# Kernel tuning notes

Hardware: AMD Instinct MI355X
Metric: run time of the kernel (lower is better)

The kernel has to match this reference:

```python
import jax, jax.numpy as jnp
import numpy as np

TAU = 0.5
EPS = 1e-12


def _projection(z, W1, b1, W2, b2):
    # fc2(elu(fc1(z)))
    h = jax.nn.elu(z @ W1 + b1)
    return h @ W2 + b2


def _l2_normalize(z):
    n = jnp.linalg.norm(z, axis=1, keepdims=True)
    return z / jnp.maximum(n, EPS)


def _semi_loss(h1, h2, tau):
    n1 = _l2_normalize(h1)
    n2 = _l2_normalize(h2)
    refl = jnp.exp((n1 @ n1.T) / tau)      # [N, N]
    between = jnp.exp((n1 @ n2.T) / tau)   # [N, N]
    denom = refl.sum(axis=1) + between.sum(axis=1) - jnp.diagonal(refl)
    return -jnp.log(jnp.diagonal(between) / denom)


def setup_inputs() -> dict:
    key = jax.random.key(0)
    k1, k2, k3, k4 = jax.random.split(key, 4)
    N, H, P = 12288, 256, 256
    s = 1.0 / np.sqrt(H)
    return {
        "z1": jax.random.normal(k1, (N, H), dtype=jnp.float32),
        "z2": jax.random.normal(k2, (N, H), dtype=jnp.float32),
        "W1": jax.random.normal(k3, (H, P), dtype=jnp.float32) * s,
        "b1": jnp.zeros((P,), dtype=jnp.float32),
        "W2": jax.random.normal(k4, (P, H), dtype=jnp.float32) * s,
        "b2": jnp.zeros((H,), dtype=jnp.float32),
    }


def reference(z1, z2, W1, b1, W2, b2):
    h1 = _projection(z1, W1, b1, W2, b2)
    h2 = _projection(z2, W1, b1, W2, b2)
    l1 = _semi_loss(h1, h2, TAU)
    l2 = _semi_loss(h2, h1, TAU)
    return ((l1 + l2) * 0.5).mean()
```

## Files before the change

### kernel.cpp

```cpp
#include <hip/hip_runtime.h>
#include <hip/hip_bf16.h>

typedef __attribute__((ext_vector_type(4))) float f32x4;
typedef __attribute__((ext_vector_type(8))) short bf16x8;

#define NR 12288
#define HD 256
#define TAU 0.5f
#define NU 24576
#define NTT 192
#define NSUB 384
#define NBLK (NTT * (NTT + 1) / 2)

__device__ __forceinline__ unsigned short f2bf(float f) {
    unsigned int x = __builtin_bit_cast(unsigned int, f);
    x += 0x7fffu + ((x >> 16) & 1u);
    return (unsigned short)(x >> 16);
}

__device__ __forceinline__ unsigned char f2e4m3(float f) {
    unsigned int u = __builtin_bit_cast(unsigned int, f);
    unsigned int s = (u >> 24) & 0x80u;
    float af = fabsf(f);
    if (af >= 464.f) return (unsigned char)(s | 0x7Eu);
    if (af < 0.015625f) {
        unsigned int q = (unsigned int)(af * 512.f + 0.5f);
        return (unsigned char)(s | q);
    }
    int e = (int)((u >> 23) & 0xffu) - 127;
    unsigned int mant = u & 0x7fffffu;
    unsigned int val = (unsigned int)((e + 7) << 3) | (mant >> 20);
    unsigned int rem = mant & 0xfffffu;
    val += (rem > 0x80000u) || (rem == 0x80000u && (val & 1u));
    return (unsigned char)(s | val);
}

__device__ __forceinline__ float row16_sum(float x) {
    int v;
    v = __builtin_amdgcn_update_dpp(0, __builtin_bit_cast(int, x), 0xB1, 0xF, 0xF, true);
    x += __builtin_bit_cast(float, v);
    v = __builtin_amdgcn_update_dpp(0, __builtin_bit_cast(int, x), 0x4E, 0xF, 0xF, true);
    x += __builtin_bit_cast(float, v);
    v = __builtin_amdgcn_update_dpp(0, __builtin_bit_cast(int, x), 0x141, 0xF, 0xF, true);
    x += __builtin_bit_cast(float, v);
    v = __builtin_amdgcn_update_dpp(0, __builtin_bit_cast(int, x), 0x140, 0xF, 0xF, true);
    x += __builtin_bit_cast(float, v);
    return x;
}

__global__ __launch_bounds__(256) void cast4_kernel(const float* __restrict__ src,
                                                    unsigned short* __restrict__ dst, int n4) {
    int i = blockIdx.x * 256 + threadIdx.x;
    if (i >= n4) return;
    float4 v = ((const float4*)src)[i];
    ushort4 u;
    u.x = f2bf(v.x); u.y = f2bf(v.y); u.z = f2bf(v.z); u.w = f2bf(v.w);
    ((ushort4*)dst)[i] = u;
}

__global__ __launch_bounds__(256) void transpose_cast_kernel(const float* __restrict__ W,
                                                             unsigned short* __restrict__ Wt) {
    int n = blockIdx.x;
    int k = threadIdx.x;
    Wt[n * HD + k] = f2bf(W[k * HD + n]);
}

template <int ELU>
__global__ __launch_bounds__(256) void proj_kernel(const unsigned short* __restrict__ A,
                                                   const unsigned short* __restrict__ Bt,
                                                   const float* __restrict__ bias,
                                                   void* __restrict__ Cout) {
    const int lane = threadIdx.x & 63;
    const int wave = threadIdx.x >> 6;
    const int row0 = blockIdx.x * 64;
    const int col0 = wave * 64;
    const int lr = lane & 15, lk = lane >> 4;

    f32x4 acc[4][4] = {};
    const unsigned short* Ab = A + (size_t)(row0 + lr) * HD + lk * 8;
    const unsigned short* Bb = Bt + (size_t)(col0 + lr) * HD + lk * 8;
#pragma unroll
    for (int k0 = 0; k0 < HD; k0 += 32) {
        bf16x8 af[4], bfr[4];
#pragma unroll
        for (int m = 0; m < 4; ++m) af[m] = *(const bf16x8*)(Ab + m * 16 * HD + k0);
#pragma unroll
        for (int n = 0; n < 4; ++n) bfr[n] = *(const bf16x8*)(Bb + n * 16 * HD + k0);
#pragma unroll
        for (int m = 0; m < 4; ++m)
#pragma unroll
            for (int n = 0; n < 4; ++n)
                acc[m][n] = __builtin_amdgcn_mfma_f32_16x16x32_bf16(af[m], bfr[n], acc[m][n], 0, 0, 0);
    }
#pragma unroll
    for (int m = 0; m < 4; ++m) {
#pragma unroll
        for (int n = 0; n < 4; ++n) {
            int col = col0 + n * 16 + lr;
            float b = bias[col];
#pragma unroll
            for (int r = 0; r < 4; ++r) {
                int row = row0 + m * 16 + lk * 4 + r;
                float v = acc[m][n][r] + b;
                if (ELU) {
                    v = v > 0.f ? v : expm1f(v);
                    ((unsigned short*)Cout)[(size_t)row * HD + col] = f2bf(v);
                } else {
                    ((float*)Cout)[(size_t)row * HD + col] = v;
                }
            }
        }
    }
}

__global__ __launch_bounds__(256) void norm_diag_kernel(const float* __restrict__ h1,
                                                        const float* __restrict__ h2,
                                                        unsigned char* __restrict__ n1,
                                                        unsigned char* __restrict__ n2,
                                                        float* __restrict__ dvec) {
    const int lane = threadIdx.x & 63;
    const int wave = threadIdx.x >> 6;
    const int row = blockIdx.x * 4 + wave;
    const float4 a = *(const float4*)(h1 + (size_t)row * HD + lane * 4);
    const float4 b = *(const float4*)(h2 + (size_t)row * HD + lane * 4);
    float sa = a.x * a.x + a.y * a.y + a.z * a.z + a.w * a.w;
    float sb = b.x * b.x + b.y * b.y + b.z * b.z + b.w * b.w;
    float sab = a.x * b.x + a.y * b.y + a.z * b.z + a.w * b.w;
#pragma unroll
    for (int m = 32; m; m >>= 1) {
        sa += __shfl_xor(sa, m);
        sb += __shfl_xor(sb, m);
        sab += __shfl_xor(sab, m);
    }
    float na = sqrtf(sa); na = na > 1e-12f ? na : 1e-12f;
    float nb = sqrtf(sb); nb = nb > 1e-12f ? nb : 1e-12f;
    float ia = 1.f / na, ib = 1.f / nb;
    uchar4 q1, q2;
    q1.x = f2e4m3(a.x * ia); q1.y = f2e4m3(a.y * ia); q1.z = f2e4m3(a.z * ia); q1.w = f2e4m3(a.w * ia);
    q2.x = f2e4m3(b.x * ib); q2.y = f2e4m3(b.y * ib); q2.z = f2e4m3(b.z * ib); q2.w = f2e4m3(b.w * ib);
    const int sw = ((row >> 3) & 1) << 3;
    *(uchar4*)(n1 + (size_t)row * HD + ((lane * 4) ^ sw)) = q1;
    *(uchar4*)(n2 + (size_t)row * HD + ((lane * 4) ^ sw)) = q2;
    if (lane == 0) dvec[row] = sab * ia * ib * (1.f / TAU);
}

__global__ __launch_bounds__(256, 2) void gram_kernel(const unsigned char* __restrict__ nU8,
                                                      float* __restrict__ RPART) {
    __shared__ __align__(16) unsigned char lA[128 * 256];
    __shared__ __align__(16) unsigned char lB[128 * 256];

    const int bid = blockIdx.x;
    const int t0 = (bid & 7) * (NBLK / 8) + (bid >> 3);
    int i = (int)((385.f - sqrtf((float)(385 * 385 - 8 * t0))) * 0.5f);
    if (i < 0) i = 0;
    if (i > NTT - 1) i = NTT - 1;
    while (i > 0 && i * NTT - i * (i - 1) / 2 > t0) --i;
    while ((i + 1) * NTT - (i + 1) * i / 2 <= t0) ++i;
    const int j = i + (t0 - (i * NTT - i * (i - 1) / 2));
    const bool diag = (i == j);

    const unsigned char* X = nU8 + (size_t)i * 128 * HD;
    const unsigned char* Y = nU8 + (size_t)j * 128 * HD;

    const int t = threadIdx.x;
    const int lane = t & 63;
    const int wave = t >> 6;
    const int wr = wave >> 1, wc = wave & 1;
    const int lr = lane & 15, lk = lane >> 4;

    {
        const int rbase = t >> 4;
        const int schunk = (t & 15) ^ rbase;
        const unsigned char* gx = X + rbase * 256 + schunk * 16;
        const unsigned char* gy = Y + rbase * 256 + schunk * 16;
#pragma unroll
        for (int c = 0; c < 8; ++c) {
            __builtin_amdgcn_global_load_lds(
                (const __attribute__((address_space(1))) unsigned int*)(gx + c * 4096),
                (__attribute__((address_space(3))) unsigned int*)(&lA[c * 4096 + t * 16]),
                16, 0, 0);
        }
        if (!diag) {
#pragma unroll
            for (int c = 0; c < 8; ++c) {
                __builtin_amdgcn_global_load_lds(
                    (const __attribute__((address_space(1))) unsigned int*)(gy + c * 4096),
                    (__attribute__((address_space(3))) unsigned int*)(&lB[c * 4096 + t * 16]),
                    16, 0, 0);
            }
        }
    }
    __syncthreads();

    f32x4 acc[4][4] = {};
    const int hswap = (lr >> 3) & 1;
    const unsigned char* sA = lA + (size_t)(wr * 64 + lr) * 256 + ((lk & 1) ^ hswap) * 8;
    const unsigned char* sBb = (diag ? lA : lB);
    const unsigned char* sB = sBb + (size_t)(wc * 64 + lr) * 256 + ((lk & 1) ^ hswap) * 8;
#pragma unroll
    for (int ks = 0; ks < 8; ++ks) {
        const int chnk = ((2 * ks + (lk >> 1)) ^ lr) * 16;
        long af[4], bfr[4];
#pragma unroll
        for (int m = 0; m < 4; ++m)
            af[m] = *(const long*)(sA + m * 16 * 256 + chnk);
#pragma unroll
        for (int n = 0; n < 4; ++n)
            bfr[n] = *(const long*)(sB + n * 16 * 256 + chnk);
#pragma unroll
        for (int m = 0; m < 4; ++m)
#pragma unroll
            for (int n = 0; n < 4; ++n)
                acc[m][n] = __builtin_amdgcn_mfma_f32_16x16x32_fp8_fp8(af[m], bfr[n], acc[m][n], 0, 0, 0);
    }

    const float kexp = 2.8853901f;
#pragma unroll
    for (int m = 0; m < 4; ++m)
#pragma unroll
        for (int n = 0; n < 4; ++n)
#pragma unroll
            for (int r = 0; r < 4; ++r)
                acc[m][n][r] = exp2f(acc[m][n][r] * kexp);

    {
        float* dst = RPART + (size_t)(2 * j + wc) * NU + i * 128 + wr * 64;
#pragma unroll
        for (int m = 0; m < 4; ++m) {
#pragma unroll
            for (int r = 0; r < 4; ++r) {
                float rs = (acc[m][0][r] + acc[m][1][r]) + (acc[m][2][r] + acc[m][3][r]);
                rs = row16_sum(rs);
                if (lr == 0) dst[m * 16 + lk * 4 + r] = rs;
            }
        }
    }
    if (!diag) {
        float* dst = RPART + (size_t)(2 * i + wr) * NU + j * 128 + wc * 64;
#pragma unroll
        for (int n = 0; n < 4; ++n) {
            float cs = 0.f;
#pragma unroll
            for (int m = 0; m < 4; ++m)
#pragma unroll
                for (int r = 0; r < 4; ++r) cs += acc[m][n][r];
            cs += __shfl_xor(cs, 16);
            cs += __shfl_xor(cs, 32);
            if (lk == 0) dst[n * 16 + lr] = cs;
        }
    }
}

__global__ __launch_bounds__(256) void reduce_part_kernel(const float* __restrict__ RPART,
                                                          float* __restrict__ S) {
    const int r = blockIdx.x * 256 + threadIdx.x;
    float s = 0.f;
#pragma unroll 8
    for (int p = 0; p < NSUB; ++p) s += RPART[(size_t)p * NU + r];
    S[r] = s;
}

__global__ __launch_bounds__(128) void loss_partial_kernel(const float* __restrict__ S,
                                                           const float* __restrict__ dvec,
                                                           float* __restrict__ partial) {
    int i = blockIdx.x * 128 + threadIdx.x;
    const float e2 = 7.389056099f;
    float d = dvec[i];
    float l1 = logf(S[i] - e2) - d;
    float l2 = logf(S[NR + i] - e2) - d;
    float v = 0.5f * (l1 + l2);
#pragma unroll
    for (int m = 32; m; m >>= 1) v += __shfl_xor(v, m);
    __shared__ float wsum[2];
    if ((threadIdx.x & 63) == 0) wsum[threadIdx.x >> 6] = v;
    __syncthreads();
    if (threadIdx.x == 0) partial[blockIdx.x] = wsum[0] + wsum[1];
}

__global__ __launch_bounds__(128) void loss_final_kernel(const float* __restrict__ partial,
                                                         float* __restrict__ out, int nb) {
    float s = 0.f;
    for (int i = threadIdx.x; i < nb; i += 128) s += partial[i];
#pragma unroll
    for (int m = 32; m; m >>= 1) s += __shfl_xor(s, m);
    __shared__ float wsum[2];
    if ((threadIdx.x & 63) == 0) wsum[threadIdx.x >> 6] = s;
    __syncthreads();
    if (threadIdx.x == 0) out[0] = (wsum[0] + wsum[1]) * (1.f / (float)NR);
}

extern "C" void kernel_launch(void* const* d_in, const int* in_sizes, int n_in,
                              void* d_out, int out_size, void* d_ws, size_t ws_size,
                              hipStream_t stream) {
    const float* z1 = (const float*)d_in[0];
    const float* z2 = (const float*)d_in[1];
    const float* W1 = (const float*)d_in[2];
    const float* b1 = (const float*)d_in[3];
    const float* W2 = (const float*)d_in[4];
    const float* b2 = (const float*)d_in[5];

    char* ws = (char*)d_ws;
    size_t off = 0;
    auto alloc = [&](size_t bytes) {
        void* p = ws + off;
        off += (bytes + 255) & ~(size_t)255;
        return p;
    };
    const size_t NH2 = (size_t)NR * HD * 2;
    unsigned short* zb1 = (unsigned short*)alloc(NH2);
    unsigned short* zb2 = (unsigned short*)alloc(NH2);
    unsigned short* W1t = (unsigned short*)alloc(HD * HD * 2);
    unsigned short* W2t = (unsigned short*)alloc(HD * HD * 2);
    unsigned short* t1 = (unsigned short*)alloc(NH2);
    unsigned short* t2 = (unsigned short*)alloc(NH2);
    float* h1 = (float*)alloc((size_t)NR * HD * 4);
    float* h2 = (float*)alloc((size_t)NR * HD * 4);
    unsigned char* nU = (unsigned char*)alloc((size_t)NU * HD);
    float* S = (float*)alloc((size_t)NU * 4);
    float* dvec = (float*)alloc(NR * 4);
    float* partial = (float*)alloc(96 * 4);
    float* RPART = (float*)ws;

    const int n4 = NR * HD / 4;
    cast4_kernel<<<(n4 + 255) / 256, 256, 0, stream>>>(z1, zb1, n4);
    cast4_kernel<<<(n4 + 255) / 256, 256, 0, stream>>>(z2, zb2, n4);
    transpose_cast_kernel<<<HD, 256, 0, stream>>>(W1, W1t);
    transpose_cast_kernel<<<HD, 256, 0, stream>>>(W2, W2t);

    proj_kernel<1><<<NR / 64, 256, 0, stream>>>(zb1, W1t, b1, t1);
    proj_kernel<1><<<NR / 64, 256, 0, stream>>>(zb2, W1t, b1, t2);
    proj_kernel<0><<<NR / 64, 256, 0, stream>>>(t1, W2t, b2, h1);
    proj_kernel<0><<<NR / 64, 256, 0, stream>>>(t2, W2t, b2, h2);

    norm_diag_kernel<<<NR / 4, 256, 0, stream>>>(h1, h2, nU, nU + (size_t)NR * HD, dvec);

    hipMemsetAsync(RPART, 0, (size_t)NSUB * NU * 4, stream);

    gram_kernel<<<NBLK, 256, 0, stream>>>(nU, RPART);

    reduce_part_kernel<<<NU / 256, 256, 0, stream>>>(RPART, S);

    loss_partial_kernel<<<NR / 128, 128, 0, stream>>>(S, dvec, partial);
    loss_final_kernel<<<1, 128, 0, stream>>>(partial, (float*)d_out, NR / 128);
}
```

Measured before the change: 293.7 us.

## Fuse cast, two-layer projection, normalization and fp8 quantization into one kernel

Replaces the two input casts, four projection GEMMs and the norm/diag kernel with one kernel per 64-row tile. It converts fp32 inputs to bf16 on the fly, keeps the ELU intermediate in swizzled LDS, and computes the norms, diagonal and fp8 quantization from registers, so the intermediate tensors never go through global memory. It also folds the exp scale into the quantization factor (sqrt of 2/(tau·ln2)), drops the RPART memset, and merges the reduce and loss-partial kernels. The trade-offs are higher register pressure (launch bounds 1), a narrower fp8 range for the pre-scaled values, and unzeroed RPART, which is only safe if the gram kernel writes every slot.

```diff
diff --git a/kernel.cpp b/kernel.cpp
--- a/kernel.cpp
+++ b/kernel.cpp
@@ -11,6 +11,7 @@
 #define NTT 192
 #define NSUB 384
 #define NBLK (NTT * (NTT + 1) / 2)
+#define LAM 1.69864368f
 
 __device__ __forceinline__ unsigned short f2bf(float f) {
     unsigned int x = __builtin_bit_cast(unsigned int, f);
@@ -48,14 +49,15 @@
     return x;
 }
 
-__global__ __launch_bounds__(256) void cast4_kernel(const float* __restrict__ src,
-                                                    unsigned short* __restrict__ dst, int n4) {
-    int i = blockIdx.x * 256 + threadIdx.x;
-    if (i >= n4) return;
-    float4 v = ((const float4*)src)[i];
-    ushort4 u;
-    u.x = f2bf(v.x); u.y = f2bf(v.y); u.z = f2bf(v.z); u.w = f2bf(v.w);
-    ((ushort4*)dst)[i] = u;
+__device__ __forceinline__ bf16x8 cvt8(const float* __restrict__ p) {
+    float4 a = *(const float4*)p;
+    float4 b = *(const float4*)(p + 4);
+    union { unsigned int i[4]; bf16x8 v; } u;
+    u.i[0] = ((unsigned int)f2bf(a.y) << 16) | f2bf(a.x);
+    u.i[1] = ((unsigned int)f2bf(a.w) << 16) | f2bf(a.z);
+    u.i[2] = ((unsigned int)f2bf(b.y) << 16) | f2bf(b.x);
+    u.i[3] = ((unsigned int)f2bf(b.w) << 16) | f2bf(b.z);
+    return u.v;
 }
 
 __global__ __launch_bounds__(256) void transpose_cast_kernel(const float* __restrict__ W,
@@ -65,83 +67,147 @@
     Wt[n * HD + k] = f2bf(W[k * HD + n]);
 }
 
-template <int ELU>
-__global__ __launch_bounds__(256) void proj_kernel(const unsigned short* __restrict__ A,
-                                                   const unsigned short* __restrict__ Bt,
-                                                   const float* __restrict__ bias,
-                                                   void* __restrict__ Cout) {
-    const int lane = threadIdx.x & 63;
-    const int wave = threadIdx.x >> 6;
+__global__ __launch_bounds__(256, 1) void fused_proj_kernel(const float* __restrict__ z1,
+                                                            const float* __restrict__ z2,
+                                                            const unsigned short* __restrict__ W1t,
+                                                            const unsigned short* __restrict__ W2t,
+                                                            const float* __restrict__ b1,
+                                                            const float* __restrict__ b2,
+                                                            unsigned char* __restrict__ nU,
+                                                            float* __restrict__ dvec) {
+    __shared__ __align__(16) unsigned char tbuf[64 * 512];
+    __shared__ float red1[4][64];
+    __shared__ float red2[4][64];
+    __shared__ float redd[4][64];
+    __shared__ float iaA[64], ibA[64];
+
+    const int t = threadIdx.x;
+    const int lane = t & 63;
+    const int wave = t >> 6;
+    const int lr = lane & 15, lk = lane >> 4;
     const int row0 = blockIdx.x * 64;
     const int col0 = wave * 64;
-    const int lr = lane & 15, lk = lane >> 4;
-
-    f32x4 acc[4][4] = {};
-    const unsigned short* Ab = A + (size_t)(row0 + lr) * HD + lk * 8;
-    const unsigned short* Bb = Bt + (size_t)(col0 + lr) * HD + lk * 8;
-#pragma unroll
-    for (int k0 = 0; k0 < HD; k0 += 32) {
-        bf16x8 af[4], bfr[4];
-#pragma unroll
-        for (int m = 0; m < 4; ++m) af[m] = *(const bf16x8*)(Ab + m * 16 * HD + k0);
-#pragma unroll
-        for (int n = 0; n < 4; ++n) bfr[n] = *(const bf16x8*)(Bb + n * 16 * HD + k0);
-#pragma unroll
-        for (int m = 0; m < 4; ++m)
-#pragma unroll
-            for (int n = 0; n < 4; ++n)
-                acc[m][n] = __builtin_amdgcn_mfma_f32_16x16x32_bf16(af[m], bfr[n], acc[m][n], 0, 0, 0);
-    }
-#pragma unroll
-    for (int m = 0; m < 4; ++m) {
-#pragma unroll
-        for (int n = 0; n < 4; ++n) {
-            int col = col0 + n * 16 + lr;
-            float b = bias[col];
+
+    float b1v[4], b2v[4];
+#pragma unroll
+    for (int n = 0; n < 4; ++n) {
+        b1v[n] = b1[col0 + n * 16 + lr];
+        b2v[n] = b2[col0 + n * 16 + lr];
+    }
+
+    f32x4 h1[4][4], h2[4][4];
+
+#pragma unroll 1
+    for (int ph = 0; ph < 2; ++ph) {
+        const float* zsrc = ph ? z2 : z1;
+        f32x4 a1[4][4] = {};
+#pragma unroll
+        for (int ks = 0; ks < 8; ++ks) {
+            bf16x8 af[4], bfr[4];
+#pragma unroll
+            for (int m = 0; m < 4; ++m)
+                af[m] = cvt8(zsrc + (size_t)(row0 + m * 16 + lr) * HD + ks * 32 + lk * 8);
+#pragma unroll
+            for (int n = 0; n < 4; ++n)
+                bfr[n] = *(const bf16x8*)(W1t + (size_t)(col0 + n * 16 + lr) * HD + ks * 32 + lk * 8);
+#pragma unroll
+            for (int m = 0; m < 4; ++m)
+#pragma unroll
+                for (int n = 0; n < 4; ++n)
+                    a1[m][n] = __builtin_amdgcn_mfma_f32_16x16x32_bf16(af[m], bfr[n], a1[m][n], 0, 0, 0);
+        }
+#pragma unroll
+        for (int m = 0; m < 4; ++m)
+#pragma unroll
+            for (int n = 0; n < 4; ++n)
+#pragma unroll
+                for (int r = 0; r < 4; ++r) {
+                    float v = a1[m][n][r] + b1v[n];
+                    v = v > 0.f ? v : expm1f(v);
+                    const int row_l = m * 16 + lk * 4 + r;
+                    const int chunk = (wave * 8 + n * 2 + (lr >> 3)) ^ (row_l & 15);
+                    *(unsigned short*)(tbuf + row_l * 512 + chunk * 16 + (lr & 7) * 2) = f2bf(v);
+                }
+        __syncthreads();
+        f32x4 a2[4][4] = {};
+#pragma unroll
+        for (int ks = 0; ks < 8; ++ks) {
+            bf16x8 af[4], bfr[4];
+#pragma unroll
+            for (int m = 0; m < 4; ++m)
+                af[m] = *(const bf16x8*)(tbuf + (m * 16 + lr) * 512 + (((ks * 4 + lk) ^ lr) * 16));
+#pragma unroll
+            for (int n = 0; n < 4; ++n)
+                bfr[n] = *(const bf16x8*)(W2t + (size_t)(col0 + n * 16 + lr) * HD + ks * 32 + lk * 8);
+#pragma unroll
+            for (int m = 0; m < 4; ++m)
+#pragma unroll
+                for (int n = 0; n < 4; ++n)
+                    a2[m][n] = __builtin_amdgcn_mfma_f32_16x16x32_bf16(af[m], bfr[n], a2[m][n], 0, 0, 0);
+        }
+#pragma unroll
+        for (int m = 0; m < 4; ++m)
+#pragma unroll
+            for (int n = 0; n < 4; ++n)
+#pragma unroll
+                for (int r = 0; r < 4; ++r) {
+                    float v = a2[m][n][r] + b2v[n];
+                    if (ph == 0) h1[m][n][r] = v; else h2[m][n][r] = v;
+                }
+#pragma unroll
+        for (int m = 0; m < 4; ++m)
 #pragma unroll
             for (int r = 0; r < 4; ++r) {
-                int row = row0 + m * 16 + lk * 4 + r;
-                float v = acc[m][n][r] + b;
-                if (ELU) {
-                    v = v > 0.f ? v : expm1f(v);
-                    ((unsigned short*)Cout)[(size_t)row * HD + col] = f2bf(v);
+                const int row_l = m * 16 + lk * 4 + r;
+                if (ph == 0) {
+                    float ss = h1[m][0][r] * h1[m][0][r] + h1[m][1][r] * h1[m][1][r] +
+                               h1[m][2][r] * h1[m][2][r] + h1[m][3][r] * h1[m][3][r];
+                    ss = row16_sum(ss);
+                    if (lr == 0) red1[wave][row_l] = ss;
                 } else {
-                    ((float*)Cout)[(size_t)row * HD + col] = v;
+                    float ss = h2[m][0][r] * h2[m][0][r] + h2[m][1][r] * h2[m][1][r] +
+                               h2[m][2][r] * h2[m][2][r] + h2[m][3][r] * h2[m][3][r];
+                    float dd = h1[m][0][r] * h2[m][0][r] + h1[m][1][r] * h2[m][1][r] +
+                               h1[m][2][r] * h2[m][2][r] + h1[m][3][r] * h2[m][3][r];
+                    ss = row16_sum(ss);
+                    dd = row16_sum(dd);
+                    if (lr == 0) { red2[wave][row_l] = ss; redd[wave][row_l] = dd; }
                 }
             }
-        }
-    }
-}
-
-__global__ __launch_bounds__(256) void norm_diag_kernel(const float* __restrict__ h1,
-                                                        const float* __restrict__ h2,
-                                                        unsigned char* __restrict__ n1,
-                                                        unsigned char* __restrict__ n2,
-                                                        float* __restrict__ dvec) {
-    const int lane = threadIdx.x & 63;
-    const int wave = threadIdx.x >> 6;
-    const int row = blockIdx.x * 4 + wave;
-    const float4 a = *(const float4*)(h1 + (size_t)row * HD + lane * 4);
-    const float4 b = *(const float4*)(h2 + (size_t)row * HD + lane * 4);
-    float sa = a.x * a.x + a.y * a.y + a.z * a.z + a.w * a.w;
-    float sb = b.x * b.x + b.y * b.y + b.z * b.z + b.w * b.w;
-    float sab = a.x * b.x + a.y * b.y + a.z * b.z + a.w * b.w;
-#pragma unroll
-    for (int m = 32; m; m >>= 1) {
-        sa += __shfl_xor(sa, m);
-        sb += __shfl_xor(sb, m);
-        sab += __shfl_xor(sab, m);
-    }
-    float na = sqrtf(sa); na = na > 1e-12f ? na : 1e-12f;
-    float nb = sqrtf(sb); nb = nb > 1e-12f ? nb : 1e-12f;
-    float ia = 1.f / na, ib = 1.f / nb;
-    uchar4 q1, q2;
-    q1.x = f2e4m3(a.x * ia); q1.y = f2e4m3(a.y * ia); q1.z = f2e4m3(a.z * ia); q1.w = f2e4m3(a.w * ia);
-    q2.x = f2e4m3(b.x * ib); q2.y = f2e4m3(b.y * ib); q2.z = f2e4m3(b.z * ib); q2.w = f2e4m3(b.w * ib);
-    const int sw = ((row >> 3) & 1) << 3;
-    *(uchar4*)(n1 + (size_t)row * HD + ((lane * 4) ^ sw)) = q1;
-    *(uchar4*)(n2 + (size_t)row * HD + ((lane * 4) ^ sw)) = q2;
-    if (lane == 0) dvec[row] = sab * ia * ib * (1.f / TAU);
+        __syncthreads();
+    }
+
+    if (t < 64) {
+        float s1 = red1[0][t] + red1[1][t] + red1[2][t] + red1[3][t];
+        float s2 = red2[0][t] + red2[1][t] + red2[2][t] + red2[3][t];
+        float dd = redd[0][t] + redd[1][t] + redd[2][t] + redd[3][t];
+        float na = sqrtf(s1); na = na > 1e-12f ? na : 1e-12f;
+        float nb = sqrtf(s2); nb = nb > 1e-12f ? nb : 1e-12f;
+        float ia = 1.f / na, ib = 1.f / nb;
+        dvec[row0 + t] = dd * ia * ib * (1.f / TAU);
+        iaA[t] = ia * LAM;
+        ibA[t] = ib * LAM;
+    }
+    __syncthreads();
+
+    unsigned char* n1p = nU;
+    unsigned char* n2p = nU + (size_t)NR * HD;
+#pragma unroll
+    for (int m = 0; m < 4; ++m)
+#pragma unroll
+        for (int r = 0; r < 4; ++r) {
+            const int row_l = m * 16 + lk * 4 + r;
+            const float iav = iaA[row_l];
+            const float ibv = ibA[row_l];
+            const int sw8 = ((row_l >> 3) & 1) << 3;
+            const size_t rb = (size_t)(row0 + row_l) * HD;
+#pragma unroll
+            for (int n = 0; n < 4; ++n) {
+                const int col = (col0 + n * 16 + lr) ^ sw8;
+                n1p[rb + col] = f2e4m3(h1[m][n][r] * iav);
+                n2p[rb + col] = f2e4m3(h2[m][n][r] * ibv);
+            }
+        }
 }
 
 __global__ __launch_bounds__(256, 2) void gram_kernel(const unsigned char* __restrict__ nU8,
@@ -214,14 +280,13 @@
                 acc[m][n] = __builtin_amdgcn_mfma_f32_16x16x32_fp8_fp8(af[m], bfr[n], acc[m][n], 0, 0, 0);
     }
 
-    const float kexp = 2.8853901f;
 #pragma unroll
     for (int m = 0; m < 4; ++m)
 #pragma unroll
         for (int n = 0; n < 4; ++n)
 #pragma unroll
             for (int r = 0; r < 4; ++r)
-                acc[m][n][r] = exp2f(acc[m][n][r] * kexp);
+                acc[m][n][r] = exp2f(acc[m][n][r]);
 
     {
         float* dst = RPART + (size_t)(2 * j + wc) * NU + i * 128 + wr * 64;
@@ -251,24 +316,18 @@
     }
 }
 
-__global__ __launch_bounds__(256) void reduce_part_kernel(const float* __restrict__ RPART,
-                                                          float* __restrict__ S) {
-    const int r = blockIdx.x * 256 + threadIdx.x;
-    float s = 0.f;
+__global__ __launch_bounds__(128) void loss_sum_kernel(const float* __restrict__ RPART,
+                                                       const float* __restrict__ dvec,
+                                                       float* __restrict__ partial) {
+    const int i = blockIdx.x * 128 + threadIdx.x;
+    float s1 = 0.f, s2 = 0.f;
 #pragma unroll 8
-    for (int p = 0; p < NSUB; ++p) s += RPART[(size_t)p * NU + r];
-    S[r] = s;
-}
-
-__global__ __launch_bounds__(128) void loss_partial_kernel(const float* __restrict__ S,
-                                                           const float* __restrict__ dvec,
-                                                           float* __restrict__ partial) {
-    int i = blockIdx.x * 128 + threadIdx.x;
+    for (int p = 0; p < NSUB; ++p) {
+        s1 += RPART[(size_t)p * NU + i];
+        s2 += RPART[(size_t)p * NU + NR + i];
+    }
     const float e2 = 7.389056099f;
-    float d = dvec[i];
-    float l1 = logf(S[i] - e2) - d;
-    float l2 = logf(S[NR + i] - e2) - d;
-    float v = 0.5f * (l1 + l2);
+    float v = 0.5f * (logf(s1 - e2) + logf(s2 - e2)) - dvec[i];
 #pragma unroll
     for (int m = 32; m; m >>= 1) v += __shfl_xor(v, m);
     __shared__ float wsum[2];
@@ -306,40 +365,20 @@
         off += (bytes + 255) & ~(size_t)255;
         return p;
     };
-    const size_t NH2 = (size_t)NR * HD * 2;
-    unsigned short* zb1 = (unsigned short*)alloc(NH2);
-    unsigned short* zb2 = (unsigned short*)alloc(NH2);
     unsigned short* W1t = (unsigned short*)alloc(HD * HD * 2);
     unsigned short* W2t = (unsigned short*)alloc(HD * HD * 2);
-    unsigned short* t1 = (unsigned short*)alloc(NH2);
-    unsigned short* t2 = (unsigned short*)alloc(NH2);
-    float* h1 = (float*)alloc((size_t)NR * HD * 4);
-    float* h2 = (float*)alloc((size_t)NR * HD * 4);
     unsigned char* nU = (unsigned char*)alloc((size_t)NU * HD);
-    float* S = (float*)alloc((size_t)NU * 4);
     float* dvec = (float*)alloc(NR * 4);
     float* partial = (float*)alloc(96 * 4);
-    float* RPART = (float*)ws;
-
-    const int n4 = NR * HD / 4;
-    cast4_kernel<<<(n4 + 255) / 256, 256, 0, stream>>>(z1, zb1, n4);
-    cast4_kernel<<<(n4 + 255) / 256, 256, 0, stream>>>(z2, zb2, n4);
+    float* RPART = (float*)alloc((size_t)NSUB * NU * 4);
+
     transpose_cast_kernel<<<HD, 256, 0, stream>>>(W1, W1t);
     transpose_cast_kernel<<<HD, 256, 0, stream>>>(W2, W2t);
 
-    proj_kernel<1><<<NR / 64, 256, 0, stream>>>(zb1, W1t, b1, t1);
-    proj_kernel<1><<<NR / 64, 256, 0, stream>>>(zb2, W1t, b1, t2);
-    proj_kernel<0><<<NR / 64, 256, 0, stream>>>(t1, W2t, b2, h1);
-    proj_kernel<0><<<NR / 64, 256, 0, stream>>>(t2, W2t, b2, h2);
-
-    norm_diag_kernel<<<NR / 4, 256, 0, stream>>>(h1, h2, nU, nU + (size_t)NR * HD, dvec);
-
-    hipMemsetAsync(RPART, 0, (size_t)NSUB * NU * 4, stream);
+    fused_proj_kernel<<<NR / 64, 256, 0, stream>>>(z1, z2, W1t, W2t, b1, b2, nU, dvec);
 
     gram_kernel<<<NBLK, 256, 0, stream>>>(nU, RPART);
 
-    reduce_part_kernel<<<NU / 256, 256, 0, stream>>>(RPART, S);
-
-    loss_partial_kernel<<<NR / 128, 128, 0, stream>>>(S, dvec, partial);
+    loss_sum_kernel<<<NR / 128, 128, 0, stream>>>(RPART, dvec, partial);
     loss_final_kernel<<<1, 128, 0, stream>>>(partial, (float*)d_out, NR / 128);
 }
```

New measurement: 308.6 us. 1.05x slower.

## Load A operand directly to registers, halve LDS, fold exp scale into quantization

Applied to the files above, without the earlier changes.

The gram kernel now reads the A tile straight from global memory into registers and stages only the B tile in LDS. This halves shared memory per block and raises the occupancy hint from 2 to 3 blocks per CU. The 1/tau·log2(e) factor is folded into the fp8 quantization scale (sqrt of the constant on each operand), which removes a multiply per exp and changes the fp8 rounding range. The memset of the partial-sum buffer is also removed, which relies on every RPART entry being written by some block.

```diff
diff --git a/kernel.cpp b/kernel.cpp
--- a/kernel.cpp
+++ b/kernel.cpp
@@ -11,6 +11,7 @@
 #define NTT 192
 #define NSUB 384
 #define NBLK (NTT * (NTT + 1) / 2)
+#define LAM 1.69864368f
 
 __device__ __forceinline__ unsigned short f2bf(float f) {
     unsigned int x = __builtin_bit_cast(unsigned int, f);
@@ -135,18 +136,18 @@
     float na = sqrtf(sa); na = na > 1e-12f ? na : 1e-12f;
     float nb = sqrtf(sb); nb = nb > 1e-12f ? nb : 1e-12f;
     float ia = 1.f / na, ib = 1.f / nb;
+    float sca = ia * LAM, scb = ib * LAM;
     uchar4 q1, q2;
-    q1.x = f2e4m3(a.x * ia); q1.y = f2e4m3(a.y * ia); q1.z = f2e4m3(a.z * ia); q1.w = f2e4m3(a.w * ia);
-    q2.x = f2e4m3(b.x * ib); q2.y = f2e4m3(b.y * ib); q2.z = f2e4m3(b.z * ib); q2.w = f2e4m3(b.w * ib);
+    q1.x = f2e4m3(a.x * sca); q1.y = f2e4m3(a.y * sca); q1.z = f2e4m3(a.z * sca); q1.w = f2e4m3(a.w * sca);
+    q2.x = f2e4m3(b.x * scb); q2.y = f2e4m3(b.y * scb); q2.z = f2e4m3(b.z * scb); q2.w = f2e4m3(b.w * scb);
     const int sw = ((row >> 3) & 1) << 3;
     *(uchar4*)(n1 + (size_t)row * HD + ((lane * 4) ^ sw)) = q1;
     *(uchar4*)(n2 + (size_t)row * HD + ((lane * 4) ^ sw)) = q2;
     if (lane == 0) dvec[row] = sab * ia * ib * (1.f / TAU);
 }
 
-__global__ __launch_bounds__(256, 2) void gram_kernel(const unsigned char* __restrict__ nU8,
+__global__ __launch_bounds__(256, 3) void gram_kernel(const unsigned char* __restrict__ nU8,
                                                       float* __restrict__ RPART) {
-    __shared__ __align__(16) unsigned char lA[128 * 256];
     __shared__ __align__(16) unsigned char lB[128 * 256];
 
     const int bid = blockIdx.x;
@@ -167,43 +168,38 @@
     const int wave = t >> 6;
     const int wr = wave >> 1, wc = wave & 1;
     const int lr = lane & 15, lk = lane >> 4;
+    const int hswap = (lr >> 3) & 1;
 
     {
         const int rbase = t >> 4;
         const int schunk = (t & 15) ^ rbase;
-        const unsigned char* gx = X + rbase * 256 + schunk * 16;
-        const unsigned char* gy = Y + rbase * 256 + schunk * 16;
+        const unsigned char* gy = (diag ? X : Y) + rbase * 256 + schunk * 16;
 #pragma unroll
         for (int c = 0; c < 8; ++c) {
             __builtin_amdgcn_global_load_lds(
-                (const __attribute__((address_space(1))) unsigned int*)(gx + c * 4096),
-                (__attribute__((address_space(3))) unsigned int*)(&lA[c * 4096 + t * 16]),
+                (const __attribute__((address_space(1))) unsigned int*)(gy + c * 4096),
+                (__attribute__((address_space(3))) unsigned int*)(&lB[c * 4096 + t * 16]),
                 16, 0, 0);
         }
-        if (!diag) {
-#pragma unroll
-            for (int c = 0; c < 8; ++c) {
-                __builtin_amdgcn_global_load_lds(
-                    (const __attribute__((address_space(1))) unsigned int*)(gy + c * 4096),
-                    (__attribute__((address_space(3))) unsigned int*)(&lB[c * 4096 + t * 16]),
-                    16, 0, 0);
-            }
-        }
+    }
+
+    long aReg[4][8];
+    {
+        const unsigned char* Abase = X + (size_t)(wr * 64 + lr) * 256 + ((lk * 8) ^ (hswap * 8));
+#pragma unroll
+        for (int m = 0; m < 4; ++m)
+#pragma unroll
+            for (int ks = 0; ks < 8; ++ks)
+                aReg[m][ks] = *(const long*)(Abase + m * 16 * 256 + ks * 32);
     }
     __syncthreads();
 
     f32x4 acc[4][4] = {};
-    const int hswap = (lr >> 3) & 1;
-    const unsigned char* sA = lA + (size_t)(wr * 64 + lr) * 256 + ((lk & 1) ^ hswap) * 8;
-    const unsigned char* sBb = (diag ? lA : lB);
-    const unsigned char* sB = sBb + (size_t)(wc * 64 + lr) * 256 + ((lk & 1) ^ hswap) * 8;
+    const unsigned char* sB = lB + (size_t)(wc * 64 + lr) * 256 + ((lk & 1) ^ hswap) * 8;
 #pragma unroll
     for (int ks = 0; ks < 8; ++ks) {
         const int chnk = ((2 * ks + (lk >> 1)) ^ lr) * 16;
-        long af[4], bfr[4];
-#pragma unroll
-        for (int m = 0; m < 4; ++m)
-            af[m] = *(const long*)(sA + m * 16 * 256 + chnk);
+        long bfr[4];
 #pragma unroll
         for (int n = 0; n < 4; ++n)
             bfr[n] = *(const long*)(sB + n * 16 * 256 + chnk);
@@ -211,17 +207,16 @@
         for (int m = 0; m < 4; ++m)
 #pragma unroll
             for (int n = 0; n < 4; ++n)
-                acc[m][n] = __builtin_amdgcn_mfma_f32_16x16x32_fp8_fp8(af[m], bfr[n], acc[m][n], 0, 0, 0);
-    }
-
-    const float kexp = 2.8853901f;
+                acc[m][n] = __builtin_amdgcn_mfma_f32_16x16x32_fp8_fp8(aReg[m][ks], bfr[n], acc[m][n], 0, 0, 0);
+    }
+
 #pragma unroll
     for (int m = 0; m < 4; ++m)
 #pragma unroll
         for (int n = 0; n < 4; ++n)
 #pragma unroll
             for (int r = 0; r < 4; ++r)
-                acc[m][n][r] = exp2f(acc[m][n][r] * kexp);
+                acc[m][n][r] = exp2f(acc[m][n][r]);
 
     {
         float* dst = RPART + (size_t)(2 * j + wc) * NU + i * 128 + wr * 64;
@@ -334,8 +329,6 @@
 
     norm_diag_kernel<<<NR / 4, 256, 0, stream>>>(h1, h2, nU, nU + (size_t)NR * HD, dvec);
 
-    hipMemsetAsync(RPART, 0, (size_t)NSUB * NU * 4, stream);
-
     gram_kernel<<<NBLK, 256, 0, stream>>>(nU, RPART);
 
     reduce_part_kernel<<<NU / 256, 256, 0, stream>>>(RPART, S);
```

Measured after the change: 385.7 us. +31.3%, slower.
